# Optimization experiments

Hardware: AMD Instinct MI355X
Metric: run time of the kernel (lower is better)

The kernel has to match this reference:

```python
import jax, jax.numpy as jnp
import numpy as np

ROUTING_ITERS = 3
EPS = 1e-07


def setup_inputs() -> dict:
    key = jax.random.key(0)
    k1, k2 = jax.random.split(key)
    B, IN_CAPS, OUT_CAPS, POSE = 128, 2048, 32, 4
    votes = jax.random.normal(k1, (B, IN_CAPS, OUT_CAPS, POSE), dtype=jnp.float32)
    activations_in = jax.random.uniform(k2, (B, IN_CAPS), dtype=jnp.float32)
    return {"votes": votes, "activations_in": activations_in}


def _safe_norm(s, axis=-1):
    # NOTE: original safe_norm always keeps dims (reduce_sum keepdims=True, then sqrt)
    return jnp.sqrt(jnp.sum(jnp.square(s), axis=axis, keepdims=True) + EPS)


def _squash(s):
    s_norm = _safe_norm(s, axis=-1)                 # [..., 1]
    scale = jnp.square(s_norm) / (1.0 + jnp.square(s_norm))
    return scale * (s / s_norm)


def reference(votes, activations_in):
    # votes: [B, in_caps, out_caps, pose]
    B, in_caps, out_caps, _ = votes.shape
    b_ij = jnp.zeros((B, in_caps, out_caps), dtype=jnp.float32)
    v_j = None
    for _ in range(ROUTING_ITERS):
        c_ij = jax.nn.softmax(b_ij, axis=2)                       # [B, I, O]
        s_j = jnp.einsum('bio,biop->bop', c_ij, votes)            # [B, O, P]
        v_j = _squash(s_j)                                        # [B, O, P]
        v_stop = jax.lax.stop_gradient(v_j)
        agreement = jnp.einsum('biop,bop->bio', votes, v_stop)    # [B, I, O]
        b_ij = b_ij + agreement
    poses_out = v_j                                               # [B, O, P]
    activations_out = _safe_norm(poses_out, axis=-1)              # [B, O, 1] (keepdims bug preserved)
    return poses_out, activations_out
```

## Files before the change

kernel.cpp:

```cpp
#include <hip/hip_runtime.h>
#include <hip/hip_fp16.h>


#define BATCH 128
#define IC 2048
#define OC 32
#define POSE 4
#define REPS 1e-7f
#define CHUNKS 16
#define CHUNK_I (IC / CHUNKS)
#define BLOCK_T 256
#define GROUPS (BLOCK_T / 32)
#define ILP 4
#define STEPS (CHUNK_I / (GROUPS * ILP))

#define PART_IDX(t, b, c, o) ((((size_t)(t) * BATCH + (b)) * CHUNKS + (c)) * OC + (o))

struct alignas(8) half4v { __half2 xy, zw; };

__device__ __forceinline__ half4v f2h(const float4 v) {
    half4v h;
    h.xy = __float22half2_rn(make_float2(v.x, v.y));
    h.zw = __float22half2_rn(make_float2(v.z, v.w));
    return h;
}
__device__ __forceinline__ float4 h2f(const half4v h) {
    const float2 a = __half22float2(h.xy);
    const float2 b = __half22float2(h.zw);
    return make_float4(a.x, a.y, b.x, b.y);
}

__device__ __forceinline__ float dot4(const float4 a, const float4 b) {
    return a.x*b.x + a.y*b.y + a.z*b.z + a.w*b.w;
}

__device__ __forceinline__ float4 squash4(const float4 s) {
    const float n2 = s.x*s.x + s.y*s.y + s.z*s.z + s.w*s.w + REPS;
    const float f = n2 / (1.f + n2) * rsqrtf(n2);
    return make_float4(f*s.x, f*s.y, f*s.z, f*s.w);
}

__device__ __forceinline__ float4 reduce_squash(
    const float4* __restrict__ partials, int t, int b, int o, float scale)
{
    float4 acc = make_float4(0.f, 0.f, 0.f, 0.f);
    #pragma unroll
    for (int c = 0; c < CHUNKS; ++c) {
        const float4 p = partials[PART_IDX(t, b, c, o)];
        acc.x += p.x; acc.y += p.y; acc.z += p.z; acc.w += p.w;
    }
    acc.x *= scale; acc.y *= scale; acc.z *= scale; acc.w *= scale;
    return squash4(acc);
}

__device__ __forceinline__ void block_reduce_store(
    float4 s_acc, float4* lds_s, float4* __restrict__ partials,
    int t, int b, int chunk, int g, int o)
{
    lds_s[g * 32 + o] = s_acc;
    __syncthreads();
    if (threadIdx.x < 32) {
        float4 tot = lds_s[o];
        #pragma unroll
        for (int gg = 1; gg < GROUPS; ++gg) {
            const float4 x = lds_s[gg * 32 + o];
            tot.x += x.x; tot.y += x.y; tot.z += x.z; tot.w += x.w;
        }
        partials[PART_IDX(t, b, chunk, o)] = tot;
    }
}

__global__ __launch_bounds__(BLOCK_T) void routing_pass0(
    const float4* __restrict__ votes,
    half4v* __restrict__ v16,
    float4* __restrict__ partials)
{
    const int blk   = blockIdx.x;
    const int b     = blk >> 4;
    const int chunk = blk & (CHUNKS - 1);
    const int o     = threadIdx.x & 31;
    const int g     = threadIdx.x >> 5;

    __shared__ float4 lds_s[GROUPS * 32];

    float4 s_acc = make_float4(0.f, 0.f, 0.f, 0.f);
    const float4* vb = votes + (size_t)b * IC * OC;
    half4v* cb = v16 + (size_t)b * IC * OC;
    const int i0 = chunk * CHUNK_I;

    #pragma unroll
    for (int step = 0; step < STEPS; ++step) {
        const int ia = i0 + step * (GROUPS * ILP) + g;
        const size_t e0 = (size_t)(ia + 0 * GROUPS) * OC + o;
        const size_t e1 = (size_t)(ia + 1 * GROUPS) * OC + o;
        const size_t e2 = (size_t)(ia + 2 * GROUPS) * OC + o;
        const size_t e3 = (size_t)(ia + 3 * GROUPS) * OC + o;
        const float4 v0 = vb[e0];
        const float4 v1 = vb[e1];
        const float4 v2 = vb[e2];
        const float4 v3 = vb[e3];

        s_acc.x += (v0.x + v1.x) + (v2.x + v3.x);
        s_acc.y += (v0.y + v1.y) + (v2.y + v3.y);
        s_acc.z += (v0.z + v1.z) + (v2.z + v3.z);
        s_acc.w += (v0.w + v1.w) + (v2.w + v3.w);

        cb[e0] = f2h(v0);
        cb[e1] = f2h(v1);
        cb[e2] = f2h(v2);
        cb[e3] = f2h(v3);
    }

    block_reduce_store(s_acc, lds_s, partials, 0, b, chunk, g, o);
}

template <int T>
__global__ __launch_bounds__(BLOCK_T) void routing_accum(
    const half4v* __restrict__ v16,
    float4* __restrict__ partials)
{
    const int blk   = blockIdx.x;
    const int b     = blk >> 4;
    const int chunk = blk & (CHUNKS - 1);
    const int o     = threadIdx.x & 31;
    const int g     = threadIdx.x >> 5;

    __shared__ float4 lds_s[GROUPS * 32];
    __shared__ float4 vh0_s[32];
    __shared__ float4 vh1_s[32];

    if (threadIdx.x < 32) {
        vh0_s[o] = reduce_squash(partials, 0, b, o, 1.f / 32.f);
        if (T >= 2) vh1_s[o] = reduce_squash(partials, 1, b, o, 1.f);
    }
    __syncthreads();
    float4 vh = vh0_s[o];
    if (T >= 2) {
        const float4 h1 = vh1_s[o];
        vh.x += h1.x; vh.y += h1.y; vh.z += h1.z; vh.w += h1.w;
    }

    float4 s_acc = make_float4(0.f, 0.f, 0.f, 0.f);
    const half4v* cb = v16 + (size_t)b * IC * OC;
    const int i0 = chunk * CHUNK_I;

    #pragma unroll
    for (int step = 0; step < STEPS; ++step) {
        const int ia = i0 + step * (GROUPS * ILP) + g;
        const float4 v0 = h2f(cb[(size_t)(ia + 0 * GROUPS) * OC + o]);
        const float4 v1 = h2f(cb[(size_t)(ia + 1 * GROUPS) * OC + o]);
        const float4 v2 = h2f(cb[(size_t)(ia + 2 * GROUPS) * OC + o]);
        const float4 v3 = h2f(cb[(size_t)(ia + 3 * GROUPS) * OC + o]);

        const float l0 = dot4(v0, vh);
        const float l1 = dot4(v1, vh);
        const float l2 = dot4(v2, vh);
        const float l3 = dot4(v3, vh);
        float e0 = __expf(l0), e1 = __expf(l1), e2 = __expf(l2), e3 = __expf(l3);
        float t0 = e0, t1 = e1, t2 = e2, t3 = e3;
        #pragma unroll
        for (int d = 16; d >= 1; d >>= 1) {
            t0 += __shfl_xor(t0, d);
            t1 += __shfl_xor(t1, d);
            t2 += __shfl_xor(t2, d);
            t3 += __shfl_xor(t3, d);
        }
        const float c0 = e0 * __builtin_amdgcn_rcpf(t0);
        const float c1 = e1 * __builtin_amdgcn_rcpf(t1);
        const float c2 = e2 * __builtin_amdgcn_rcpf(t2);
        const float c3 = e3 * __builtin_amdgcn_rcpf(t3);

        s_acc.x += c0*v0.x + c1*v1.x + c2*v2.x + c3*v3.x;
        s_acc.y += c0*v0.y + c1*v1.y + c2*v2.y + c3*v3.y;
        s_acc.z += c0*v0.z + c1*v1.z + c2*v2.z + c3*v3.z;
        s_acc.w += c0*v0.w + c1*v1.w + c2*v2.w + c3*v3.w;
    }

    __syncthreads();
    block_reduce_store(s_acc, lds_s, partials, T, b, chunk, g, o);
}

__global__ void routing_finalize(
    const float4* __restrict__ partials,
    float* __restrict__ out)
{
    const int idx = blockIdx.x * blockDim.x + threadIdx.x;
    if (idx >= BATCH * OC) return;
    const int b = idx >> 5, o = idx & 31;
    const float4 v = reduce_squash(partials, 2, b, o, 1.f);
    ((float4*)out)[idx] = v;
    const float a = sqrtf(v.x*v.x + v.y*v.y + v.z*v.z + v.w*v.w + REPS);
    out[BATCH * OC * POSE + idx] = a;
}

extern "C" void kernel_launch(void* const* d_in, const int* in_sizes, int n_in,
                              void* d_out, int out_size, void* d_ws, size_t ws_size,
                              hipStream_t stream) {
    const float4* votes = (const float4*)d_in[0];

    float4* partials = (float4*)d_ws;
    half4v* v16 = (half4v*)((char*)d_ws + (size_t)3 * BATCH * CHUNKS * OC * sizeof(float4));

    routing_pass0<<<BATCH * CHUNKS, BLOCK_T, 0, stream>>>(votes, v16, partials);
    routing_accum<1><<<BATCH * CHUNKS, BLOCK_T, 0, stream>>>(v16, partials);
    routing_accum<2><<<BATCH * CHUNKS, BLOCK_T, 0, stream>>>(v16, partials);
    routing_finalize<<<(BATCH * OC + 255) / 256, 256, 0, stream>>>(
        partials, (float*)d_out);
}
```

Baseline: 230.7 us.

## Fuse routing passes into one persistent kernel with per-batch atomic barriers

```diff
diff --git a/kernel.cpp b/kernel.cpp
--- a/kernel.cpp
+++ b/kernel.cpp
@@ -7,12 +7,13 @@
 #define OC 32
 #define POSE 4
 #define REPS 1e-7f
-#define CHUNKS 16
+#define CHUNKS 8
 #define CHUNK_I (IC / CHUNKS)
 #define BLOCK_T 256
 #define GROUPS (BLOCK_T / 32)
 #define ILP 4
 #define STEPS (CHUNK_I / (GROUPS * ILP))
+#define SLOTS (STEPS * ILP)
 
 #define PART_IDX(t, b, c, o) ((((size_t)(t) * BATCH + (b)) * CHUNKS + (c)) * OC + (o))
 
@@ -70,87 +71,32 @@
     }
 }
 
-__global__ __launch_bounds__(BLOCK_T) void routing_pass0(
-    const float4* __restrict__ votes,
-    half4v* __restrict__ v16,
-    float4* __restrict__ partials)
-{
-    const int blk   = blockIdx.x;
-    const int b     = blk >> 4;
-    const int chunk = blk & (CHUNKS - 1);
-    const int o     = threadIdx.x & 31;
-    const int g     = threadIdx.x >> 5;
-
-    __shared__ float4 lds_s[GROUPS * 32];
-
+__device__ __forceinline__ void bar_arrive(unsigned int* cnt) {
+    __syncthreads();
+    if (threadIdx.x == 0) {
+        __threadfence();
+        __hip_atomic_fetch_add(cnt, 1u, __ATOMIC_RELEASE, __HIP_MEMORY_SCOPE_AGENT);
+    }
+}
+__device__ __forceinline__ void bar_wait(unsigned int* cnt, unsigned int target) {
+    if (threadIdx.x == 0) {
+        while (__hip_atomic_load(cnt, __ATOMIC_ACQUIRE, __HIP_MEMORY_SCOPE_AGENT) < target)
+            __builtin_amdgcn_s_sleep(2);
+        __threadfence();
+    }
+    __syncthreads();
+}
+
+__device__ __forceinline__ float4 accum_pass(const half4v* __restrict__ hv,
+                                             const float4 vh)
+{
     float4 s_acc = make_float4(0.f, 0.f, 0.f, 0.f);
-    const float4* vb = votes + (size_t)b * IC * OC;
-    half4v* cb = v16 + (size_t)b * IC * OC;
-    const int i0 = chunk * CHUNK_I;
-
     #pragma unroll
     for (int step = 0; step < STEPS; ++step) {
-        const int ia = i0 + step * (GROUPS * ILP) + g;
-        const size_t e0 = (size_t)(ia + 0 * GROUPS) * OC + o;
-        const size_t e1 = (size_t)(ia + 1 * GROUPS) * OC + o;
-        const size_t e2 = (size_t)(ia + 2 * GROUPS) * OC + o;
-        const size_t e3 = (size_t)(ia + 3 * GROUPS) * OC + o;
-        const float4 v0 = vb[e0];
-        const float4 v1 = vb[e1];
-        const float4 v2 = vb[e2];
-        const float4 v3 = vb[e3];
-
-        s_acc.x += (v0.x + v1.x) + (v2.x + v3.x);
-        s_acc.y += (v0.y + v1.y) + (v2.y + v3.y);
-        s_acc.z += (v0.z + v1.z) + (v2.z + v3.z);
-        s_acc.w += (v0.w + v1.w) + (v2.w + v3.w);
-
-        cb[e0] = f2h(v0);
-        cb[e1] = f2h(v1);
-        cb[e2] = f2h(v2);
-        cb[e3] = f2h(v3);
-    }
-
-    block_reduce_store(s_acc, lds_s, partials, 0, b, chunk, g, o);
-}
-
-template <int T>
-__global__ __launch_bounds__(BLOCK_T) void routing_accum(
-    const half4v* __restrict__ v16,
-    float4* __restrict__ partials)
-{
-    const int blk   = blockIdx.x;
-    const int b     = blk >> 4;
-    const int chunk = blk & (CHUNKS - 1);
-    const int o     = threadIdx.x & 31;
-    const int g     = threadIdx.x >> 5;
-
-    __shared__ float4 lds_s[GROUPS * 32];
-    __shared__ float4 vh0_s[32];
-    __shared__ float4 vh1_s[32];
-
-    if (threadIdx.x < 32) {
-        vh0_s[o] = reduce_squash(partials, 0, b, o, 1.f / 32.f);
-        if (T >= 2) vh1_s[o] = reduce_squash(partials, 1, b, o, 1.f);
-    }
-    __syncthreads();
-    float4 vh = vh0_s[o];
-    if (T >= 2) {
-        const float4 h1 = vh1_s[o];
-        vh.x += h1.x; vh.y += h1.y; vh.z += h1.z; vh.w += h1.w;
-    }
-
-    float4 s_acc = make_float4(0.f, 0.f, 0.f, 0.f);
-    const half4v* cb = v16 + (size_t)b * IC * OC;
-    const int i0 = chunk * CHUNK_I;
-
-    #pragma unroll
-    for (int step = 0; step < STEPS; ++step) {
-        const int ia = i0 + step * (GROUPS * ILP) + g;
-        const float4 v0 = h2f(cb[(size_t)(ia + 0 * GROUPS) * OC + o]);
-        const float4 v1 = h2f(cb[(size_t)(ia + 1 * GROUPS) * OC + o]);
-        const float4 v2 = h2f(cb[(size_t)(ia + 2 * GROUPS) * OC + o]);
-        const float4 v3 = h2f(cb[(size_t)(ia + 3 * GROUPS) * OC + o]);
+        const float4 v0 = h2f(hv[step * ILP + 0]);
+        const float4 v1 = h2f(hv[step * ILP + 1]);
+        const float4 v2 = h2f(hv[step * ILP + 2]);
+        const float4 v3 = h2f(hv[step * ILP + 3]);
 
         const float l0 = dot4(v0, vh);
         const float l1 = dot4(v1, vh);
@@ -175,22 +121,78 @@
         s_acc.z += c0*v0.z + c1*v1.z + c2*v2.z + c3*v3.z;
         s_acc.w += c0*v0.w + c1*v1.w + c2*v2.w + c3*v3.w;
     }
-
-    __syncthreads();
-    block_reduce_store(s_acc, lds_s, partials, T, b, chunk, g, o);
-}
-
-__global__ void routing_finalize(
-    const float4* __restrict__ partials,
-    float* __restrict__ out)
-{
-    const int idx = blockIdx.x * blockDim.x + threadIdx.x;
-    if (idx >= BATCH * OC) return;
-    const int b = idx >> 5, o = idx & 31;
-    const float4 v = reduce_squash(partials, 2, b, o, 1.f);
-    ((float4*)out)[idx] = v;
-    const float a = sqrtf(v.x*v.x + v.y*v.y + v.z*v.z + v.w*v.w + REPS);
-    out[BATCH * OC * POSE + idx] = a;
+    return s_acc;
+}
+
+__global__ void routing_init(unsigned int* __restrict__ counters) {
+    if (threadIdx.x < BATCH) counters[threadIdx.x * 32] = 0;
+}
+
+__global__ __launch_bounds__(BLOCK_T, 4) void routing_fused(
+    const float4* __restrict__ votes,
+    float* __restrict__ out,
+    unsigned int* __restrict__ counters,
+    float4* __restrict__ partials)
+{
+    const int blk   = blockIdx.x;
+    const int b     = blk >> 3;
+    const int chunk = blk & (CHUNKS - 1);
+    const int o     = threadIdx.x & 31;
+    const int g     = threadIdx.x >> 5;
+    unsigned int* cnt = counters + (size_t)b * 32;
+
+    __shared__ float4 lds_s[GROUPS * 32];
+    __shared__ float4 vh_s[32];
+
+    half4v hv[SLOTS];
+    const float4* vb = votes + (size_t)b * IC * OC;
+    const int i0 = chunk * CHUNK_I;
+
+    float4 s_acc = make_float4(0.f, 0.f, 0.f, 0.f);
+    #pragma unroll
+    for (int step = 0; step < STEPS; ++step) {
+        const int ia = i0 + step * (GROUPS * ILP) + g;
+        const float4* vp = vb + (size_t)ia * OC + o;
+        #pragma unroll
+        for (int k = 0; k < ILP; ++k) {
+            const float4 v = vp[(size_t)k * GROUPS * OC];
+            hv[step * ILP + k] = f2h(v);
+            s_acc.x += v.x; s_acc.y += v.y; s_acc.z += v.z; s_acc.w += v.w;
+        }
+    }
+    block_reduce_store(s_acc, lds_s, partials, 0, b, chunk, g, o);
+    bar_arrive(cnt);
+    bar_wait(cnt, 1 * CHUNKS);
+
+    if (threadIdx.x < 32)
+        vh_s[o] = reduce_squash(partials, 0, b, o, 1.f / 32.f);
+    __syncthreads();
+    const float4 vh0 = vh_s[o];
+
+    const float4 s1 = accum_pass(hv, vh0);
+    block_reduce_store(s1, lds_s, partials, 1, b, chunk, g, o);
+    bar_arrive(cnt);
+    bar_wait(cnt, 2 * CHUNKS);
+
+    if (threadIdx.x < 32)
+        vh_s[o] = reduce_squash(partials, 1, b, o, 1.f);
+    __syncthreads();
+    float4 vh01 = vh_s[o];
+    vh01.x += vh0.x; vh01.y += vh0.y; vh01.z += vh0.z; vh01.w += vh0.w;
+
+    const float4 s2 = accum_pass(hv, vh01);
+    block_reduce_store(s2, lds_s, partials, 2, b, chunk, g, o);
+    bar_arrive(cnt);
+
+    if (chunk == 0) {
+        bar_wait(cnt, 3 * CHUNKS);
+        if (threadIdx.x < 32) {
+            const float4 v = reduce_squash(partials, 2, b, o, 1.f);
+            ((float4*)out)[b * OC + o] = v;
+            const float a = sqrtf(v.x*v.x + v.y*v.y + v.z*v.z + v.w*v.w + REPS);
+            out[BATCH * OC * POSE + b * OC + o] = a;
+        }
+    }
 }
 
 extern "C" void kernel_launch(void* const* d_in, const int* in_sizes, int n_in,
@@ -198,12 +200,10 @@
                               hipStream_t stream) {
     const float4* votes = (const float4*)d_in[0];
 
-    float4* partials = (float4*)d_ws;
-    half4v* v16 = (half4v*)((char*)d_ws + (size_t)3 * BATCH * CHUNKS * OC * sizeof(float4));
-
-    routing_pass0<<<BATCH * CHUNKS, BLOCK_T, 0, stream>>>(votes, v16, partials);
-    routing_accum<1><<<BATCH * CHUNKS, BLOCK_T, 0, stream>>>(v16, partials);
-    routing_accum<2><<<BATCH * CHUNKS, BLOCK_T, 0, stream>>>(v16, partials);
-    routing_finalize<<<(BATCH * OC + 255) / 256, 256, 0, stream>>>(
-        partials, (float*)d_out);
-}
+    unsigned int* counters = (unsigned int*)d_ws;
+    float4* partials = (float4*)((char*)d_ws + 16 * 1024);
+
+    routing_init<<<1, 128, 0, stream>>>(counters);
+    routing_fused<<<BATCH * CHUNKS, BLOCK_T, 0, stream>>>(
+        votes, (float*)d_out, counters, partials);
+}
```

New measurement: 641.0 us. 178% more time.

## Fold finalize and per-batch reduction into last-arriving block via atomic counters

Applied to the files above, without the earlier changes.

```diff
diff --git a/kernel.cpp b/kernel.cpp
--- a/kernel.cpp
+++ b/kernel.cpp
@@ -70,80 +70,22 @@
     }
 }
 
-__global__ __launch_bounds__(BLOCK_T) void routing_pass0(
-    const float4* __restrict__ votes,
-    half4v* __restrict__ v16,
-    float4* __restrict__ partials)
-{
-    const int blk   = blockIdx.x;
-    const int b     = blk >> 4;
-    const int chunk = blk & (CHUNKS - 1);
-    const int o     = threadIdx.x & 31;
-    const int g     = threadIdx.x >> 5;
-
-    __shared__ float4 lds_s[GROUPS * 32];
-
+__device__ __forceinline__ bool fanin_last(unsigned int* cnt, int* last_s) {
+    __syncthreads();
+    if (threadIdx.x == 0) {
+        __threadfence();
+        const unsigned old = __hip_atomic_fetch_add(
+            cnt, 1u, __ATOMIC_ACQ_REL, __HIP_MEMORY_SCOPE_AGENT);
+        *last_s = (old == CHUNKS - 1);
+    }
+    __syncthreads();
+    return *last_s != 0;
+}
+
+__device__ __forceinline__ float4 pass_accum(
+    const half4v* __restrict__ cb, int i0, int g, int o, const float4 vh)
+{
     float4 s_acc = make_float4(0.f, 0.f, 0.f, 0.f);
-    const float4* vb = votes + (size_t)b * IC * OC;
-    half4v* cb = v16 + (size_t)b * IC * OC;
-    const int i0 = chunk * CHUNK_I;
-
-    #pragma unroll
-    for (int step = 0; step < STEPS; ++step) {
-        const int ia = i0 + step * (GROUPS * ILP) + g;
-        const size_t e0 = (size_t)(ia + 0 * GROUPS) * OC + o;
-        const size_t e1 = (size_t)(ia + 1 * GROUPS) * OC + o;
-        const size_t e2 = (size_t)(ia + 2 * GROUPS) * OC + o;
-        const size_t e3 = (size_t)(ia + 3 * GROUPS) * OC + o;
-        const float4 v0 = vb[e0];
-        const float4 v1 = vb[e1];
-        const float4 v2 = vb[e2];
-        const float4 v3 = vb[e3];
-
-        s_acc.x += (v0.x + v1.x) + (v2.x + v3.x);
-        s_acc.y += (v0.y + v1.y) + (v2.y + v3.y);
-        s_acc.z += (v0.z + v1.z) + (v2.z + v3.z);
-        s_acc.w += (v0.w + v1.w) + (v2.w + v3.w);
-
-        cb[e0] = f2h(v0);
-        cb[e1] = f2h(v1);
-        cb[e2] = f2h(v2);
-        cb[e3] = f2h(v3);
-    }
-
-    block_reduce_store(s_acc, lds_s, partials, 0, b, chunk, g, o);
-}
-
-template <int T>
-__global__ __launch_bounds__(BLOCK_T) void routing_accum(
-    const half4v* __restrict__ v16,
-    float4* __restrict__ partials)
-{
-    const int blk   = blockIdx.x;
-    const int b     = blk >> 4;
-    const int chunk = blk & (CHUNKS - 1);
-    const int o     = threadIdx.x & 31;
-    const int g     = threadIdx.x >> 5;
-
-    __shared__ float4 lds_s[GROUPS * 32];
-    __shared__ float4 vh0_s[32];
-    __shared__ float4 vh1_s[32];
-
-    if (threadIdx.x < 32) {
-        vh0_s[o] = reduce_squash(partials, 0, b, o, 1.f / 32.f);
-        if (T >= 2) vh1_s[o] = reduce_squash(partials, 1, b, o, 1.f);
-    }
-    __syncthreads();
-    float4 vh = vh0_s[o];
-    if (T >= 2) {
-        const float4 h1 = vh1_s[o];
-        vh.x += h1.x; vh.y += h1.y; vh.z += h1.z; vh.w += h1.w;
-    }
-
-    float4 s_acc = make_float4(0.f, 0.f, 0.f, 0.f);
-    const half4v* cb = v16 + (size_t)b * IC * OC;
-    const int i0 = chunk * CHUNK_I;
-
     #pragma unroll
     for (int step = 0; step < STEPS; ++step) {
         const int ia = i0 + step * (GROUPS * ILP) + g;
@@ -175,22 +117,119 @@
         s_acc.z += c0*v0.z + c1*v1.z + c2*v2.z + c3*v3.z;
         s_acc.w += c0*v0.w + c1*v1.w + c2*v2.w + c3*v3.w;
     }
-
-    __syncthreads();
-    block_reduce_store(s_acc, lds_s, partials, T, b, chunk, g, o);
-}
-
-__global__ void routing_finalize(
-    const float4* __restrict__ partials,
-    float* __restrict__ out)
-{
-    const int idx = blockIdx.x * blockDim.x + threadIdx.x;
-    if (idx >= BATCH * OC) return;
-    const int b = idx >> 5, o = idx & 31;
-    const float4 v = reduce_squash(partials, 2, b, o, 1.f);
-    ((float4*)out)[idx] = v;
-    const float a = sqrtf(v.x*v.x + v.y*v.y + v.z*v.z + v.w*v.w + REPS);
-    out[BATCH * OC * POSE + idx] = a;
+    return s_acc;
+}
+
+__global__ __launch_bounds__(BLOCK_T) void routing_t0(
+    const float4* __restrict__ votes,
+    half4v* __restrict__ v16,
+    float4* __restrict__ partials,
+    unsigned int* __restrict__ counters)
+{
+    if (blockIdx.x == 0) counters[threadIdx.x * 32] = 0;
+
+    const int blk   = blockIdx.x;
+    const int b     = blk >> 4;
+    const int chunk = blk & (CHUNKS - 1);
+    const int o     = threadIdx.x & 31;
+    const int g     = threadIdx.x >> 5;
+
+    __shared__ float4 lds_s[GROUPS * 32];
+
+    float4 s_acc = make_float4(0.f, 0.f, 0.f, 0.f);
+    const float4* vb = votes + (size_t)b * IC * OC;
+    half4v* cb = v16 + (size_t)b * IC * OC;
+    const int i0 = chunk * CHUNK_I;
+
+    #pragma unroll
+    for (int step = 0; step < STEPS; ++step) {
+        const int ia = i0 + step * (GROUPS * ILP) + g;
+        const size_t e0 = (size_t)(ia + 0 * GROUPS) * OC + o;
+        const size_t e1 = (size_t)(ia + 1 * GROUPS) * OC + o;
+        const size_t e2 = (size_t)(ia + 2 * GROUPS) * OC + o;
+        const size_t e3 = (size_t)(ia + 3 * GROUPS) * OC + o;
+        const float4 v0 = vb[e0];
+        const float4 v1 = vb[e1];
+        const float4 v2 = vb[e2];
+        const float4 v3 = vb[e3];
+
+        s_acc.x += (v0.x + v1.x) + (v2.x + v3.x);
+        s_acc.y += (v0.y + v1.y) + (v2.y + v3.y);
+        s_acc.z += (v0.z + v1.z) + (v2.z + v3.z);
+        s_acc.w += (v0.w + v1.w) + (v2.w + v3.w);
+
+        cb[e0] = f2h(v0);
+        cb[e1] = f2h(v1);
+        cb[e2] = f2h(v2);
+        cb[e3] = f2h(v3);
+    }
+
+    block_reduce_store(s_acc, lds_s, partials, 0, b, chunk, g, o);
+}
+
+__global__ __launch_bounds__(BLOCK_T) void routing_t1(
+    const half4v* __restrict__ v16,
+    float4* __restrict__ partials,
+    float4* __restrict__ vsum,
+    unsigned int* __restrict__ counters)
+{
+    const int blk   = blockIdx.x;
+    const int b     = blk >> 4;
+    const int chunk = blk & (CHUNKS - 1);
+    const int o     = threadIdx.x & 31;
+    const int g     = threadIdx.x >> 5;
+
+    __shared__ float4 lds_s[GROUPS * 32];
+    __shared__ float4 vh_s[32];
+    __shared__ int    last_s;
+
+    if (threadIdx.x < 32)
+        vh_s[o] = reduce_squash(partials, 0, b, o, 1.f / 32.f);
+    __syncthreads();
+    const float4 vh0 = vh_s[o];
+
+    const float4 s1 = pass_accum(v16 + (size_t)b * IC * OC, chunk * CHUNK_I, g, o, vh0);
+    __syncthreads();
+    block_reduce_store(s1, lds_s, partials, 1, b, chunk, g, o);
+
+    if (fanin_last(&counters[b * 32], &last_s)) {
+        if (threadIdx.x < 32) {
+            const float4 v1 = reduce_squash(partials, 1, b, o, 1.f);
+            vsum[b * OC + o] = make_float4(vh0.x + v1.x, vh0.y + v1.y,
+                                           vh0.z + v1.z, vh0.w + v1.w);
+        }
+    }
+}
+
+__global__ __launch_bounds__(BLOCK_T) void routing_t2(
+    const half4v* __restrict__ v16,
+    float4* __restrict__ partials,
+    const float4* __restrict__ vsum,
+    float* __restrict__ out,
+    unsigned int* __restrict__ counters)
+{
+    const int blk   = blockIdx.x;
+    const int b     = blk >> 4;
+    const int chunk = blk & (CHUNKS - 1);
+    const int o     = threadIdx.x & 31;
+    const int g     = threadIdx.x >> 5;
+
+    __shared__ float4 lds_s[GROUPS * 32];
+    __shared__ int    last_s;
+
+    const float4 vh01 = vsum[b * OC + o];
+
+    const float4 s2 = pass_accum(v16 + (size_t)b * IC * OC, chunk * CHUNK_I, g, o, vh01);
+    block_reduce_store(s2, lds_s, partials, 2, b, chunk, g, o);
+
+    if (fanin_last(&counters[(BATCH + b) * 32], &last_s)) {
+        if (threadIdx.x < 32) {
+            const float4 v = reduce_squash(partials, 2, b, o, 1.f);
+            ((float4*)out)[b * OC + o] = v;
+            const float a = sqrtf(v.x*v.x + v.y*v.y + v.z*v.z + v.w*v.w + REPS);
+            out[BATCH * OC * POSE + b * OC + o] = a;
+        }
+    }
 }
 
 extern "C" void kernel_launch(void* const* d_in, const int* in_sizes, int n_in,
@@ -198,12 +237,13 @@
                               hipStream_t stream) {
     const float4* votes = (const float4*)d_in[0];
 
-    float4* partials = (float4*)d_ws;
-    half4v* v16 = (half4v*)((char*)d_ws + (size_t)3 * BATCH * CHUNKS * OC * sizeof(float4));
-
-    routing_pass0<<<BATCH * CHUNKS, BLOCK_T, 0, stream>>>(votes, v16, partials);
-    routing_accum<1><<<BATCH * CHUNKS, BLOCK_T, 0, stream>>>(v16, partials);
-    routing_accum<2><<<BATCH * CHUNKS, BLOCK_T, 0, stream>>>(v16, partials);
-    routing_finalize<<<(BATCH * OC + 255) / 256, 256, 0, stream>>>(
-        partials, (float*)d_out);
-}
+    unsigned int* counters = (unsigned int*)d_ws;
+    float4* partials = (float4*)((char*)d_ws + 32 * 1024);
+    float4* vsum     = (float4*)((char*)d_ws + 32 * 1024 + (size_t)3 * 1024 * 1024);
+    half4v* v16      = (half4v*)((char*)d_ws + (size_t)4 * 1024 * 1024);
+
+    routing_t0<<<BATCH * CHUNKS, BLOCK_T, 0, stream>>>(votes, v16, partials, counters);
+    routing_t1<<<BATCH * CHUNKS, BLOCK_T, 0, stream>>>(v16, partials, vsum, counters);
+    routing_t2<<<BATCH * CHUNKS, BLOCK_T, 0, stream>>>(v16, partials, vsum,
+                                                       (float*)d_out, counters);
+}
```

Result: slower. 409.3 us (+77.4%).
